# Performance work log

Measured on AMD Instinct MI355X. Metric: run time of the kernel, lower is better.

The kernel has to match this reference:

```python
import jax, jax.numpy as jnp
import numpy as np

N_NODES = 100000
N_EDGES = 1280000
D_IN = 64
D_OUT = 64


def setup_inputs() -> dict:
    key = jax.random.key(0)
    k_x, k_e, k_w, k_rw = jax.random.split(key, 4)
    x = jax.random.normal(k_x, (N_NODES, D_IN), dtype=jnp.float32)
    edge_index = jax.random.randint(k_e, (2, N_EDGES), 0, N_NODES, dtype=jnp.int32)
    glorot = float(np.sqrt(6.0 / (D_IN + D_OUT)))
    weight = jax.random.uniform(k_w, (D_IN, D_OUT), dtype=jnp.float32, minval=-glorot, maxval=glorot)
    root_weight = jax.random.uniform(k_rw, (D_IN, D_OUT), dtype=jnp.float32, minval=-glorot, maxval=glorot)
    bias = jnp.zeros((D_OUT,), dtype=jnp.float32)
    return {"x": x, "edge_index": edge_index, "weight": weight,
            "root_weight": root_weight, "bias": bias}


def reference(x, edge_index, weight, root_weight, bias):
    # adj_0 = SparseTensor(row=edge_index[0], col=edge_index[1])
    # adj_0.matmul(x, reduce='mean'): out[i] = mean_{(i,j) in E} x[j]
    n = x.shape[0]
    row, col = edge_index[0], edge_index[1]
    msg = x[col]                                              # [E, D_in] gather
    summed = jax.ops.segment_sum(msg, row, num_segments=n)    # [N, D_in]
    count = jax.ops.segment_sum(jnp.ones((row.shape[0],), dtype=x.dtype), row,
                                num_segments=n)               # [N]
    agg = summed / jnp.maximum(count, 1.0)[:, None]           # mean (deg-0 -> 0)
    out = agg @ weight + x @ root_weight + bias
    return out
```

## Files before the change

### kernel.cpp

```cpp
#include <hip/hip_runtime.h>
#include <hip/hip_bf16.h>

#define N_NODES 100000
#define N_EDGES 1280000
#define D 64
#define NB ((N_NODES + 255) / 256)
#define NBKT 391
#define BKT_SHIFT 8
#define BKT_NODES 256
#define CAP 3712
#define HBKT 782
#define HALF_PAD 2048
#define BIN_EPB 4096
#define BIN_BLOCKS 313
#define PRE_BLOCKS 782

using short8 = __attribute__((ext_vector_type(8))) short;
using f32x4  = __attribute__((ext_vector_type(4))) float;

__device__ __forceinline__ unsigned short f2bf(float f) {
    unsigned int u = __float_as_uint(f);
    unsigned int r = (u + 0x7FFFu + ((u >> 16) & 1u)) >> 16;
    return (unsigned short)r;
}

__device__ __forceinline__ float bf2f(unsigned short u) {
    union { unsigned int i; float f; } v;
    v.i = ((unsigned int)u) << 16;
    return v.f;
}


__global__ void zero_bcnt_kernel(int* __restrict__ bcnt) {
    int t = threadIdx.x;
    if (t < NBKT) bcnt[t] = 0;
}

__launch_bounds__(512)
__global__ void bin_pre_kernel(const int* __restrict__ row,
                               const int* __restrict__ col,
                               int* __restrict__ bucket_cnt,
                               unsigned int* __restrict__ pairs,
                               const float* __restrict__ x,
                               const float* __restrict__ W,
                               const float* __restrict__ Wr,
                               const float* __restrict__ bias,
                               unsigned int* __restrict__ y_packed,
                               float* __restrict__ out) {
    __shared__ __align__(16) char smem[22784];
    int tid = threadIdx.x;

    if (blockIdx.x < BIN_BLOCKS) {
        unsigned int* sorted = (unsigned int*)smem;
        int* cnt   = (int*)(smem + 16384);
        int* lexcl = cnt + NBKT;
        int* lcur  = lexcl + NBKT;
        int* gbase = lcur + NBKT;
        int* wsum  = gbase + NBKT;
        int* wexcl = wsum + 8;

        for (int i = tid; i < NBKT; i += 512) cnt[i] = 0;
        __syncthreads();

        int rr[8], cc[8];
#pragma unroll
        for (int i = 0; i < 8; ++i) {
            int e = blockIdx.x * BIN_EPB + i * 512 + tid;
            if (e < N_EDGES) {
                rr[i] = row[e];
                cc[i] = col[e];
                atomicAdd(&cnt[rr[i] >> BKT_SHIFT], 1);
            } else {
                rr[i] = -1;
            }
        }
        __syncthreads();

        int lane = tid & 63, wv = tid >> 6;
        int v = (tid < NBKT) ? cnt[tid] : 0;
        int incl = v;
#pragma unroll
        for (int d = 1; d < 64; d <<= 1) {
            int u = __shfl_up(incl, d, 64);
            if (lane >= d) incl += u;
        }
        if (lane == 63) wsum[wv] = incl;
        __syncthreads();
        if (tid < 8) {
            int w = wsum[tid];
            int p = w;
#pragma unroll
            for (int d = 1; d < 8; d <<= 1) {
                int u = __shfl_up(p, d, 64);
                if (tid >= d) p += u;
            }
            wexcl[tid] = p - w;
        }
        __syncthreads();
        if (tid < NBKT) {
            int excl = incl - v + wexcl[wv];
            lexcl[tid] = excl;
            lcur[tid]  = excl;
            if (v > 0) gbase[tid] = atomicAdd(&bucket_cnt[tid], v);
        }
        __syncthreads();

#pragma unroll
        for (int i = 0; i < 8; ++i) {
            if (rr[i] >= 0) {
                int b = rr[i] >> BKT_SHIFT;
                int slot = atomicAdd(&lcur[b], 1);
                sorted[slot] = ((unsigned int)(rr[i] & (BKT_NODES - 1)) << 17)
                             | (unsigned int)cc[i];
            }
        }
        __syncthreads();

        int grp = tid >> 4, l16 = tid & 15;
        for (int bb = grp; bb < NBKT; bb += 32) {
            int len = cnt[bb];
            if (len == 0) continue;
            int src = lexcl[bb];
            int dst = gbase[bb];
            for (int k = l16; k < len; k += 16) {
                int gs = dst + k;
                if (gs < CAP)
                    pairs[(size_t)bb * CAP + gs] = sorted[src + k];
            }
        }
    } else {
        unsigned short* Wl = (unsigned short*)smem;

        for (int idx = tid; idx < 8192; idx += 512) {
            int j    = idx & 7;
            int lane = (idx >> 3) & 63;
            int h    = (idx >> 9) & 1;
            int t    = (idx >> 10) & 3;
            int mat  = idx >> 12;
            int k = h * 32 + ((lane >> 4) << 3) + j;
            int n = t * 16 + (lane & 15);
            const float* src = mat ? Wr : W;
            Wl[idx] = f2bf(src[k * D + n]);
        }
        __syncthreads();

        int wv = tid >> 6;
        int lane = tid & 63;
        int g = (blockIdx.x - BIN_BLOCKS) * 8 + wv;
        if (g >= N_NODES / 16) return;

        int quad = lane >> 4;
        int n16 = lane & 15;
        int m_node = g * 16 + n16;

        short8 A[2];
#pragma unroll
        for (int h = 0; h < 2; ++h) {
            const float* xr = x + (size_t)m_node * D + h * 32 + quad * 8;
            float4 xa = *(const float4*)xr;
            float4 xb = *(const float4*)(xr + 4);
            short8 a;
            a[0] = (short)f2bf(xa.x); a[1] = (short)f2bf(xa.y);
            a[2] = (short)f2bf(xa.z); a[3] = (short)f2bf(xa.w);
            a[4] = (short)f2bf(xb.x); a[5] = (short)f2bf(xb.y);
            a[6] = (short)f2bf(xb.z); a[7] = (short)f2bf(xb.w);
            A[h] = a;
        }

        int row0 = g * 16 + quad * 4;

#pragma unroll
        for (int t = 0; t < 4; ++t) {
            short8 By0 = *(const short8*)&Wl[(((0 * 4 + t) * 2 + 0) * 64 + lane) * 8];
            short8 By1 = *(const short8*)&Wl[(((0 * 4 + t) * 2 + 1) * 64 + lane) * 8];
            short8 Bz0 = *(const short8*)&Wl[(((1 * 4 + t) * 2 + 0) * 64 + lane) * 8];
            short8 Bz1 = *(const short8*)&Wl[(((1 * 4 + t) * 2 + 1) * 64 + lane) * 8];

            f32x4 accY = {0.f, 0.f, 0.f, 0.f};
            accY = __builtin_amdgcn_mfma_f32_16x16x32_bf16(A[0], By0, accY, 0, 0, 0);
            accY = __builtin_amdgcn_mfma_f32_16x16x32_bf16(A[1], By1, accY, 0, 0, 0);
            f32x4 accZ = {0.f, 0.f, 0.f, 0.f};
            accZ = __builtin_amdgcn_mfma_f32_16x16x32_bf16(A[0], Bz0, accZ, 0, 0, 0);
            accZ = __builtin_amdgcn_mfma_f32_16x16x32_bf16(A[1], Bz1, accZ, 0, 0, 0);

            float bv = bias[t * 16 + n16];
#pragma unroll
            for (int r = 0; r < 4; ++r) {
                out[(size_t)(row0 + r) * D + t * 16 + n16] = accZ[r] + bv;
                unsigned int me = f2bf(accY[r]);
                unsigned int nb = (unsigned int)__shfl_xor((int)me, 1, 64) & 0xFFFFu;
                if ((lane & 1) == 0)
                    y_packed[((size_t)(row0 + r) * D + t * 16 + n16) >> 1] = me | (nb << 16);
            }
        }
    }
}

__launch_bounds__(512, 4)
__global__ void csr_gather_kernel(const unsigned short* __restrict__ yu,
                                  const unsigned int* __restrict__ pairs,
                                  const int* __restrict__ bucket_cnt,
                                  float* __restrict__ out) {
    __shared__ int col_lds[HALF_PAD];
    __shared__ int deg_s[128];
    __shared__ int start_s[128];
    __shared__ int lcur[128];
    __shared__ int cnt_s[128];
    __shared__ int wsum[2];

    int bb = blockIdx.x;
    int b = bb >> 1;
    int rbase = (bb & 1) << 7;
    int tid = threadIdx.x;
    int m = bucket_cnt[b];
    if (m > CAP) m = CAP;
    const uint4* pb4 = (const uint4*)(pairs + (size_t)b * CAP);

    if (tid < 128) cnt_s[tid] = 0;
    __syncthreads();

    uint4 pa = pb4[tid];
    uint4 pc = (tid < CAP / 4 - 512) ? pb4[tid + 512] : make_uint4(0u, 0u, 0u, 0u);
    int ea = 4 * tid, ec = 2048 + 4 * tid;
    bool a0 = ea + 0 < m, a1 = ea + 1 < m, a2 = ea + 2 < m, a3 = ea + 3 < m;
    bool c0 = ec + 0 < m, c1 = ec + 1 < m, c2 = ec + 2 < m, c3 = ec + 3 < m;

#define CNT(p, v) if (v) { int r = (int)((p) >> 17) - rbase; \
                           if ((unsigned)r < 128u) atomicAdd(&cnt_s[r], 1); }
    CNT(pa.x, a0) CNT(pa.y, a1) CNT(pa.z, a2) CNT(pa.w, a3)
    CNT(pc.x, c0) CNT(pc.y, c1) CNT(pc.z, c2) CNT(pc.w, c3)
#undef CNT
    __syncthreads();

    if (tid < 128) {
        int v = cnt_s[tid];
        int incl = v;
        for (int d = 1; d < 64; d <<= 1) {
            int t = __shfl_up(incl, d, 64);
            if ((tid & 63) >= d) incl += t;
        }
        if ((tid & 63) == 63) wsum[tid >> 6] = incl;
        deg_s[tid] = v;
        cnt_s[tid] = incl;
    }
    __syncthreads();
    if (tid < 128) {
        int pre = (tid >= 64) ? wsum[0] : 0;
        int excl = cnt_s[tid] + pre - deg_s[tid];
        start_s[tid] = excl;
        lcur[tid] = excl;
    }
    __syncthreads();

#define SCAT(p, v) if (v) { int r = (int)((p) >> 17) - rbase; \
                            if ((unsigned)r < 128u) { \
                                int c = (int)((p) & 0x1FFFFu); \
                                col_lds[atomicAdd(&lcur[r], 1) & (HALF_PAD - 1)] = \
                                    c < N_NODES ? c : 0; } }
    SCAT(pa.x, a0) SCAT(pa.y, a1) SCAT(pa.z, a2) SCAT(pa.w, a3)
    SCAT(pc.x, c0) SCAT(pc.y, c1) SCAT(pc.z, c2) SCAT(pc.w, c3)
#undef SCAT
    __syncthreads();

    int wv = tid >> 6;
    int lane = tid & 63;
    int s = lane >> 4;
    int q = lane & 15;

#pragma unroll 1
    for (int pk = 0; pk < 4; ++pk) {
        int n0 = wv * 16 + pk * 4;
        int nvx = deg_s[n0 + 0], nvy = deg_s[n0 + 1],
            nvz = deg_s[n0 + 2], nvw = deg_s[n0 + 3];
        int st0 = start_s[n0 + 0], st1 = start_s[n0 + 1],
            st2 = start_s[n0 + 2], st3 = start_s[n0 + 3];

        float4 a0v = make_float4(0.f, 0.f, 0.f, 0.f);
        float4 a1v = a0v, a2v = a0v, a3v = a0v;

        {
            int mm = nvx > nvy ? nvx : nvy;
            for (int j = 0; j < mm; j += 4) {
                int jj = j + s;
                int c0i = col_lds[(st0 + jj) & (HALF_PAD - 1)];
                int c1i = col_lds[(st1 + jj) & (HALF_PAD - 1)];
                c0i = (jj < nvx) ? c0i : 0;
                c1i = (jj < nvy) ? c1i : 0;
                ushort4 u0 = *(const ushort4*)&yu[(size_t)c0i * D + q * 4];
                ushort4 u1 = *(const ushort4*)&yu[(size_t)c1i * D + q * 4];
                if (jj < nvx) {
                    a0v.x += bf2f(u0.x); a0v.y += bf2f(u0.y);
                    a0v.z += bf2f(u0.z); a0v.w += bf2f(u0.w);
                }
                if (jj < nvy) {
                    a1v.x += bf2f(u1.x); a1v.y += bf2f(u1.y);
                    a1v.z += bf2f(u1.z); a1v.w += bf2f(u1.w);
                }
            }
        }
        {
            int mm = nvz > nvw ? nvz : nvw;
            for (int j = 0; j < mm; j += 4) {
                int jj = j + s;
                int c2i = col_lds[(st2 + jj) & (HALF_PAD - 1)];
                int c3i = col_lds[(st3 + jj) & (HALF_PAD - 1)];
                c2i = (jj < nvz) ? c2i : 0;
                c3i = (jj < nvw) ? c3i : 0;
                ushort4 u2 = *(const ushort4*)&yu[(size_t)c2i * D + q * 4];
                ushort4 u3 = *(const ushort4*)&yu[(size_t)c3i * D + q * 4];
                if (jj < nvz) {
                    a2v.x += bf2f(u2.x); a2v.y += bf2f(u2.y);
                    a2v.z += bf2f(u2.z); a2v.w += bf2f(u2.w);
                }
                if (jj < nvw) {
                    a3v.x += bf2f(u3.x); a3v.y += bf2f(u3.y);
                    a3v.z += bf2f(u3.z); a3v.w += bf2f(u3.w);
                }
            }
        }

#define BFLY(a) \
    a.x += __shfl_xor(a.x, 16, 64); a.y += __shfl_xor(a.y, 16, 64); \
    a.z += __shfl_xor(a.z, 16, 64); a.w += __shfl_xor(a.w, 16, 64); \
    a.x += __shfl_xor(a.x, 32, 64); a.y += __shfl_xor(a.y, 32, 64); \
    a.z += __shfl_xor(a.z, 32, 64); a.w += __shfl_xor(a.w, 32, 64);
        BFLY(a0v) BFLY(a1v) BFLY(a2v) BFLY(a3v)
#undef BFLY

        float inv0 = 1.0f / (float)(nvx > 1 ? nvx : 1);
        float inv1 = 1.0f / (float)(nvy > 1 ? nvy : 1);
        float inv2 = 1.0f / (float)(nvz > 1 ? nvz : 1);
        float inv3 = 1.0f / (float)(nvw > 1 ? nvw : 1);

        float4 rr = (s == 0) ? a0v : (s == 1) ? a1v : (s == 2) ? a2v : a3v;
        float invs = (s == 0) ? inv0 : (s == 1) ? inv1 : (s == 2) ? inv2 : inv3;
        int g = (b << BKT_SHIFT) + rbase + n0 + s;
        if (g < N_NODES) {
            size_t off = (size_t)g * D + q * 4;
            float4 z = *(const float4*)&out[off];
            z.x += rr.x * invs; z.y += rr.y * invs;
            z.z += rr.z * invs; z.w += rr.w * invs;
            *(float4*)&out[off] = z;
        }
    }
}


__global__ void hist_kernel(const int4* __restrict__ row4, int* __restrict__ deg) {
    int t = blockIdx.x * blockDim.x + threadIdx.x;
    if (t < N_EDGES / 4) {
        int4 r = row4[t];
        atomicAdd(&deg[r.x], 1);
        atomicAdd(&deg[r.y], 1);
        atomicAdd(&deg[r.z], 1);
        atomicAdd(&deg[r.w], 1);
    }
}

__global__ void scan_block_kernel(const int* __restrict__ deg,
                                  int* __restrict__ cursor,
                                  int* __restrict__ bsum) {
    __shared__ int s[256];
    int tid = threadIdx.x;
    int gid = blockIdx.x * 256 + tid;
    int v = (gid < N_NODES) ? deg[gid] : 0;
    s[tid] = v;
    __syncthreads();
    for (int d = 1; d < 256; d <<= 1) {
        int t = (tid >= d) ? s[tid - d] : 0;
        __syncthreads();
        s[tid] += t;
        __syncthreads();
    }
    if (gid < N_NODES) cursor[gid] = s[tid] - v;
    if (tid == 255) bsum[blockIdx.x] = s[255];
}

__global__ void add_offsets_kernel(int* __restrict__ cursor,
                                   const int* __restrict__ bsum_raw) {
    __shared__ int red[256];
    int tid = threadIdx.x;
    int b = blockIdx.x;
    int sum = 0;
    for (int i = tid; i < b; i += 256) sum += bsum_raw[i];
    red[tid] = sum;
    __syncthreads();
    for (int off = 128; off > 0; off >>= 1) {
        if (tid < off) red[tid] += red[tid + off];
        __syncthreads();
    }
    int gid = b * 256 + tid;
    if (gid < N_NODES) cursor[gid] += red[0];
}

__global__ void scatter_build_kernel(const int4* __restrict__ row4,
                                     const int4* __restrict__ col4,
                                     int* __restrict__ cursor,
                                     int* __restrict__ col_sorted) {
    int t = blockIdx.x * blockDim.x + threadIdx.x;
    if (t < N_EDGES / 4) {
        int4 r = row4[t];
        int4 c = col4[t];
        col_sorted[atomicAdd(&cursor[r.x], 1)] = c.x;
        col_sorted[atomicAdd(&cursor[r.y], 1)] = c.y;
        col_sorted[atomicAdd(&cursor[r.z], 1)] = c.z;
        col_sorted[atomicAdd(&cursor[r.w], 1)] = c.w;
    }
}

__launch_bounds__(512, 8)
__global__ void aggregate_kernel(const float* __restrict__ x,
                                 const int* __restrict__ cursor_end,
                                 const int* __restrict__ deg,
                                 const int* __restrict__ col_sorted,
                                 const float* __restrict__ W,
                                 const float* __restrict__ Wr,
                                 const float* __restrict__ bias,
                                 float* __restrict__ out) {
    __shared__ float Ws[D * D];
    __shared__ float Wrs[D * D];
    __shared__ float agg_s[8][D];
    __shared__ float x_s[8][D];

    for (int i = threadIdx.x; i < D * D / 4; i += 512) {
        ((float4*)Ws)[i]  = ((const float4*)W)[i];
        ((float4*)Wrs)[i] = ((const float4*)Wr)[i];
    }
    __syncthreads();

    int wv = threadIdx.x >> 6;
    int lane = threadIdx.x & 63;
    int s = lane >> 4;
    int q = lane & 15;
    float bf = bias[lane];

    int node0 = (blockIdx.x * 8 + wv) * 4;

#pragma unroll 1
    for (int nn = 0; nn < 4; ++nn) {
        int r = node0 + nn;
        int n = deg[r];
        int start = cursor_end[r] - n;

        float4 acc = make_float4(0.f, 0.f, 0.f, 0.f);
        for (int base = 0; base < n; base += 64) {
            int m = n - base; if (m > 64) m = 64;
            int idx = 0;
            if (lane < m) idx = col_sorted[start + base + lane];
            for (int j = 0; j < m; j += 4) {
                int jj = j + s;
                int c = __shfl(idx, jj, 64);
                if (jj < m) {
                    float4 v = *(const float4*)&x[(size_t)c * D + q * 4];
                    acc.x += v.x; acc.y += v.y; acc.z += v.z; acc.w += v.w;
                }
            }
        }
        acc.x += __shfl_xor(acc.x, 16, 64);
        acc.y += __shfl_xor(acc.y, 16, 64);
        acc.z += __shfl_xor(acc.z, 16, 64);
        acc.w += __shfl_xor(acc.w, 16, 64);
        acc.x += __shfl_xor(acc.x, 32, 64);
        acc.y += __shfl_xor(acc.y, 32, 64);
        acc.z += __shfl_xor(acc.z, 32, 64);
        acc.w += __shfl_xor(acc.w, 32, 64);

        float inv = 1.0f / (float)(n > 1 ? n : 1);
        if (lane < 16) {
            float4 a = make_float4(acc.x * inv, acc.y * inv, acc.z * inv, acc.w * inv);
            *(float4*)&agg_s[wv][q * 4] = a;
            *(float4*)&x_s[wv][q * 4] = *(const float4*)&x[(size_t)r * D + q * 4];
        }
        __builtin_amdgcn_wave_barrier();

        int f = lane;
        float o = bf;
        const float4* av = (const float4*)agg_s[wv];
        const float4* xv = (const float4*)x_s[wv];
#pragma unroll
        for (int k4 = 0; k4 < 16; ++k4) {
            float4 a = av[k4];
            float4 xx = xv[k4];
            int k = k4 * 4;
            o += a.x * Ws[(k + 0) * D + f] + xx.x * Wrs[(k + 0) * D + f];
            o += a.y * Ws[(k + 1) * D + f] + xx.y * Wrs[(k + 1) * D + f];
            o += a.z * Ws[(k + 2) * D + f] + xx.z * Wrs[(k + 2) * D + f];
            o += a.w * Ws[(k + 3) * D + f] + xx.w * Wrs[(k + 3) * D + f];
        }
        out[(size_t)r * D + f] = o;
        __builtin_amdgcn_wave_barrier();
    }
}


__global__ void zero_kernel(float* __restrict__ summed, float* __restrict__ cnt) {
    int stride = gridDim.x * blockDim.x;
    int i = blockIdx.x * blockDim.x + threadIdx.x;
    const int total = N_NODES * D;
    for (int idx = i; idx < total; idx += stride) summed[idx] = 0.0f;
    for (int idx = i; idx < N_NODES; idx += stride) cnt[idx] = 0.0f;
}

__global__ void scatter_atomic_kernel(const float* __restrict__ x,
                                      const int* __restrict__ row,
                                      const int* __restrict__ col,
                                      float* __restrict__ summed,
                                      float* __restrict__ cnt) {
    long long gid = (long long)blockIdx.x * blockDim.x + threadIdx.x;
    const long long total = (long long)N_EDGES * D;
    if (gid >= total) return;
    int e = (int)(gid >> 6);
    int f = (int)(gid & 63);
    int r = row[e];
    int c = col[e];
    atomicAdd(&summed[r * D + f], x[c * D + f]);
    if (f == 0) atomicAdd(&cnt[r], 1.0f);
}

__global__ void finish_kernel(const float* __restrict__ x,
                              const float* __restrict__ W,
                              const float* __restrict__ Wr,
                              const float* __restrict__ bias,
                              const float* __restrict__ cnt,
                              float* __restrict__ out) {
    __shared__ float agg_s[4][D];
    __shared__ float x_s[4][D];
    int lrow = threadIdx.x >> 6;
    int f = threadIdx.x & 63;
    int r = blockIdx.x * 4 + lrow;

    float c = cnt[r];
    float inv = 1.0f / fmaxf(c, 1.0f);
    agg_s[lrow][f] = out[r * D + f] * inv;
    x_s[lrow][f] = x[r * D + f];
    __syncthreads();

    float acc = bias[f];
#pragma unroll 8
    for (int k = 0; k < D; ++k) {
        acc += agg_s[lrow][k] * W[k * D + f];
        acc += x_s[lrow][k] * Wr[k * D + f];
    }
    out[r * D + f] = acc;
}


extern "C" void kernel_launch(void* const* d_in, const int* in_sizes, int n_in,
                              void* d_out, int out_size, void* d_ws, size_t ws_size,
                              hipStream_t stream) {
    const float* x    = (const float*)d_in[0];
    const int*   ei   = (const int*)d_in[1];
    const float* W    = (const float*)d_in[2];
    const float* Wr   = (const float*)d_in[3];
    const float* bias = (const float*)d_in[4];
    float* out = (float*)d_out;

    const int* row = ei;
    const int* col = ei + N_EDGES;

    const size_t t1_cnt   = 0;
    const size_t t1_pairs = 2048;
    const size_t t1_y     = 2048 + (size_t)NBKT * CAP * 4;
    const size_t t1_need  = t1_y + (size_t)N_NODES * D * 2;

    const size_t csr_bytes = (size_t)2 * N_NODES * 4 + 2048 + (size_t)N_EDGES * 4;

    if (ws_size >= t1_need) {
        char* ws = (char*)d_ws;
        int* bcnt = (int*)(ws + t1_cnt);
        unsigned int* pairs    = (unsigned int*)(ws + t1_pairs);
        unsigned int* y_packed = (unsigned int*)(ws + t1_y);

        zero_bcnt_kernel<<<1, 512, 0, stream>>>(bcnt);
        bin_pre_kernel<<<BIN_BLOCKS + PRE_BLOCKS, 512, 0, stream>>>(
            row, col, bcnt, pairs, x, W, Wr, bias, y_packed, out);
        csr_gather_kernel<<<HBKT, 512, 0, stream>>>(
            (const unsigned short*)y_packed, pairs, bcnt, out);
    } else if (ws_size >= csr_bytes) {
        char* ws = (char*)d_ws;
        int* deg        = (int*)(ws);
        int* cursor     = (int*)(ws + (size_t)1 * N_NODES * 4);
        int* bsum       = (int*)(ws + (size_t)2 * N_NODES * 4);
        int* col_sorted = (int*)(ws + (size_t)2 * N_NODES * 4 + 2048);

        hipMemsetAsync(deg, 0, (size_t)N_NODES * 4, stream);
        hist_kernel<<<(N_EDGES / 4 + 255) / 256, 256, 0, stream>>>((const int4*)row, deg);
        scan_block_kernel<<<NB, 256, 0, stream>>>(deg, cursor, bsum);
        add_offsets_kernel<<<NB, 256, 0, stream>>>(cursor, bsum);
        scatter_build_kernel<<<(N_EDGES / 4 + 255) / 256, 256, 0, stream>>>(
            (const int4*)row, (const int4*)col, cursor, col_sorted);
        aggregate_kernel<<<N_NODES / 32, 512, 0, stream>>>(x, cursor, deg, col_sorted, W, Wr, bias, out);
    } else {
        float* cnt = (float*)d_ws;
        zero_kernel<<<4096, 256, 0, stream>>>(out, cnt);
        long long total = (long long)N_EDGES * D;
        int blocks = (int)((total + 255) / 256);
        scatter_atomic_kernel<<<blocks, 256, 0, stream>>>(x, row, col, out, cnt);
        finish_kernel<<<(N_NODES + 3) / 4, 256, 0, stream>>>(x, W, Wr, bias, cnt, out);
    }
}
```

Measured before the change: 141.7 us.

## Move root-weight matmul into gather kernel to avoid out round-trip

The x@Wr+bias term is no longer computed in the pre kernel and written to out. The gather kernel now computes it per block with MFMA into shared memory, then writes the final result once. This removes one full write and one read of the output array, roughly 51 MB of traffic. In exchange each gather block converts Wr to bf16 in LDS, which is redundant across blocks, and shared-memory use rises, which may lower occupancy.

New measurement: 154.9 us. +9.3%, slower.

```diff
diff --git a/kernel.cpp b/kernel.cpp
--- a/kernel.cpp
+++ b/kernel.cpp
@@ -11,6 +11,7 @@
 #define CAP 3712
 #define HBKT 782
 #define HALF_PAD 2048
+#define ZSTRIDE 68
 #define BIN_EPB 4096
 #define BIN_BLOCKS 313
 #define PRE_BLOCKS 782
@@ -43,10 +44,7 @@
                                unsigned int* __restrict__ pairs,
                                const float* __restrict__ x,
                                const float* __restrict__ W,
-                               const float* __restrict__ Wr,
-                               const float* __restrict__ bias,
-                               unsigned int* __restrict__ y_packed,
-                               float* __restrict__ out) {
+                               unsigned int* __restrict__ y_packed) {
     __shared__ __align__(16) char smem[22784];
     int tid = threadIdx.x;
 
@@ -131,16 +129,14 @@
     } else {
         unsigned short* Wl = (unsigned short*)smem;
 
-        for (int idx = tid; idx < 8192; idx += 512) {
+        for (int idx = tid; idx < 4096; idx += 512) {
             int j    = idx & 7;
             int lane = (idx >> 3) & 63;
             int h    = (idx >> 9) & 1;
             int t    = (idx >> 10) & 3;
-            int mat  = idx >> 12;
             int k = h * 32 + ((lane >> 4) << 3) + j;
             int n = t * 16 + (lane & 15);
-            const float* src = mat ? Wr : W;
-            Wl[idx] = f2bf(src[k * D + n]);
+            Wl[idx] = f2bf(W[k * D + n]);
         }
         __syncthreads();
 
@@ -171,22 +167,15 @@
 
 #pragma unroll
         for (int t = 0; t < 4; ++t) {
-            short8 By0 = *(const short8*)&Wl[(((0 * 4 + t) * 2 + 0) * 64 + lane) * 8];
-            short8 By1 = *(const short8*)&Wl[(((0 * 4 + t) * 2 + 1) * 64 + lane) * 8];
-            short8 Bz0 = *(const short8*)&Wl[(((1 * 4 + t) * 2 + 0) * 64 + lane) * 8];
-            short8 Bz1 = *(const short8*)&Wl[(((1 * 4 + t) * 2 + 1) * 64 + lane) * 8];
+            short8 By0 = *(const short8*)&Wl[(((t * 2 + 0) * 64 + lane) * 8)];
+            short8 By1 = *(const short8*)&Wl[(((t * 2 + 1) * 64 + lane) * 8)];
 
             f32x4 accY = {0.f, 0.f, 0.f, 0.f};
             accY = __builtin_amdgcn_mfma_f32_16x16x32_bf16(A[0], By0, accY, 0, 0, 0);
             accY = __builtin_amdgcn_mfma_f32_16x16x32_bf16(A[1], By1, accY, 0, 0, 0);
-            f32x4 accZ = {0.f, 0.f, 0.f, 0.f};
-            accZ = __builtin_amdgcn_mfma_f32_16x16x32_bf16(A[0], Bz0, accZ, 0, 0, 0);
-            accZ = __builtin_amdgcn_mfma_f32_16x16x32_bf16(A[1], Bz1, accZ, 0, 0, 0);
-
-            float bv = bias[t * 16 + n16];
+
 #pragma unroll
             for (int r = 0; r < 4; ++r) {
-                out[(size_t)(row0 + r) * D + t * 16 + n16] = accZ[r] + bv;
                 unsigned int me = f2bf(accY[r]);
                 unsigned int nb = (unsigned int)__shfl_xor((int)me, 1, 64) & 0xFFFFu;
                 if ((lane & 1) == 0)
@@ -200,6 +189,9 @@
 __global__ void csr_gather_kernel(const unsigned short* __restrict__ yu,
                                   const unsigned int* __restrict__ pairs,
                                   const int* __restrict__ bucket_cnt,
+                                  const float* __restrict__ x,
+                                  const float* __restrict__ Wr,
+                                  const float* __restrict__ bias,
                                   float* __restrict__ out) {
     __shared__ int col_lds[HALF_PAD];
     __shared__ int deg_s[128];
@@ -207,6 +199,8 @@
     __shared__ int lcur[128];
     __shared__ int cnt_s[128];
     __shared__ int wsum[2];
+    __shared__ unsigned short Wrl[4096];
+    __shared__ __align__(16) float z_s[8][16][ZSTRIDE];
 
     int bb = blockIdx.x;
     int b = bb >> 1;
@@ -216,6 +210,15 @@
     if (m > CAP) m = CAP;
     const uint4* pb4 = (const uint4*)(pairs + (size_t)b * CAP);
 
+    for (int idx = tid; idx < 4096; idx += 512) {
+        int j    = idx & 7;
+        int lane = (idx >> 3) & 63;
+        int h    = (idx >> 9) & 1;
+        int t    = (idx >> 10) & 3;
+        int k = h * 32 + ((lane >> 4) << 3) + j;
+        int n = t * 16 + (lane & 15);
+        Wrl[idx] = f2bf(Wr[k * D + n]);
+    }
     if (tid < 128) cnt_s[tid] = 0;
     __syncthreads();
 
@@ -224,6 +227,43 @@
     int ea = 4 * tid, ec = 2048 + 4 * tid;
     bool a0 = ea + 0 < m, a1 = ea + 1 < m, a2 = ea + 2 < m, a3 = ea + 3 < m;
     bool c0 = ec + 0 < m, c1 = ec + 1 < m, c2 = ec + 2 < m, c3 = ec + 3 < m;
+
+    int wv = tid >> 6;
+    int lane = tid & 63;
+    int quad = lane >> 4;
+    int n16 = lane & 15;
+
+    {
+        int m_node = (b << BKT_SHIFT) + rbase + wv * 16 + n16;
+        if (m_node >= N_NODES) m_node = N_NODES - 1;
+        short8 A[2];
+#pragma unroll
+        for (int h = 0; h < 2; ++h) {
+            const float* xr = x + (size_t)m_node * D + h * 32 + quad * 8;
+            float4 xa = *(const float4*)xr;
+            float4 xb = *(const float4*)(xr + 4);
+            short8 a;
+            a[0] = (short)f2bf(xa.x); a[1] = (short)f2bf(xa.y);
+            a[2] = (short)f2bf(xa.z); a[3] = (short)f2bf(xa.w);
+            a[4] = (short)f2bf(xb.x); a[5] = (short)f2bf(xb.y);
+            a[6] = (short)f2bf(xb.z); a[7] = (short)f2bf(xb.w);
+            A[h] = a;
+        }
+#pragma unroll
+        for (int t = 0; t < 4; ++t) {
+            short8 Bz0 = *(const short8*)&Wrl[(((t * 2 + 0) * 64 + lane) * 8)];
+            short8 Bz1 = *(const short8*)&Wrl[(((t * 2 + 1) * 64 + lane) * 8)];
+
+            f32x4 accZ = {0.f, 0.f, 0.f, 0.f};
+            accZ = __builtin_amdgcn_mfma_f32_16x16x32_bf16(A[0], Bz0, accZ, 0, 0, 0);
+            accZ = __builtin_amdgcn_mfma_f32_16x16x32_bf16(A[1], Bz1, accZ, 0, 0, 0);
+
+            float bv = bias[t * 16 + n16];
+#pragma unroll
+            for (int r = 0; r < 4; ++r)
+                z_s[wv][quad * 4 + r][t * 16 + n16] = accZ[r] + bv;
+        }
+    }
 
 #define CNT(p, v) if (v) { int r = (int)((p) >> 17) - rbase; \
                            if ((unsigned)r < 128u) atomicAdd(&cnt_s[r], 1); }
@@ -262,8 +302,6 @@
 #undef SCAT
     __syncthreads();
 
-    int wv = tid >> 6;
-    int lane = tid & 63;
     int s = lane >> 4;
     int q = lane & 15;
 
@@ -336,11 +374,12 @@
         float invs = (s == 0) ? inv0 : (s == 1) ? inv1 : (s == 2) ? inv2 : inv3;
         int g = (b << BKT_SHIFT) + rbase + n0 + s;
         if (g < N_NODES) {
+            float4 zz = *(const float4*)&z_s[wv][pk * 4 + s][q * 4];
+            float4 res;
+            res.x = zz.x + rr.x * invs; res.y = zz.y + rr.y * invs;
+            res.z = zz.z + rr.z * invs; res.w = zz.w + rr.w * invs;
             size_t off = (size_t)g * D + q * 4;
-            float4 z = *(const float4*)&out[off];
-            z.x += rr.x * invs; z.y += rr.y * invs;
-            z.z += rr.z * invs; z.w += rr.w * invs;
-            *(float4*)&out[off] = z;
+            *(float4*)&out[off] = res;
         }
     }
 }
@@ -573,9 +612,9 @@
 
         zero_bcnt_kernel<<<1, 512, 0, stream>>>(bcnt);
         bin_pre_kernel<<<BIN_BLOCKS + PRE_BLOCKS, 512, 0, stream>>>(
-            row, col, bcnt, pairs, x, W, Wr, bias, y_packed, out);
+            row, col, bcnt, pairs, x, W, y_packed);
         csr_gather_kernel<<<HBKT, 512, 0, stream>>>(
-            (const unsigned short*)y_packed, pairs, bcnt, out);
+            (const unsigned short*)y_packed, pairs, bcnt, x, Wr, bias, out);
     } else if (ws_size >= csr_bytes) {
         char* ws = (char*)d_ws;
         int* deg        = (int*)(ws);
```
